# Performance work log

Hardware: AMD Instinct MI355X
Metric: run time of the kernel (lower is better)

## Reference

```python
import jax, jax.numpy as jnp
import numpy as np

B, CIN, COUT, G, HEADS = 4, 256, 256, 8, 4
K, S, P = 7, 1, 3
H = W = 32
IN_W = CIN // G
OUT_W = COUT // G


def setup_inputs() -> dict:
    key = jax.random.key(0)
    ks = jax.random.split(key, 9)
    def n(k, shape, scale=1.0):
        return jax.random.normal(k, shape, dtype=jnp.float32) * scale
    # kaiming fan_out init for the 1x1 convs (fan_out = out channels)
    return {
        "x": n(ks[0], (B, CIN, H, W)),
        "wq": n(ks[1], (G, OUT_W * HEADS, IN_W), (2.0 / (OUT_W * HEADS)) ** 0.5),
        "bq": n(ks[2], (G, OUT_W * HEADS), 0.01),
        "wk": n(ks[3], (G, OUT_W, IN_W), (2.0 / OUT_W) ** 0.5),
        "bk": n(ks[4], (G, OUT_W), 0.01),
        "wv": n(ks[5], (G, OUT_W, IN_W), (2.0 / OUT_W) ** 0.5),
        "bv": n(ks[6], (G, OUT_W), 0.01),
        "rel_h": n(ks[7], (OUT_W // 2, 1, 1, G, K, 1)),
        "rel_w": n(ks[8], (OUT_W // 2, 1, 1, G, 1, K)),
    }


def _sparse_conv(x, w, b):
    # grouped 1x1 conv, groups stacked on last axis (matches torch.stack(dim=-1))
    # x: [B, G*I, h, w]; w: [G, O, I]; b: [G, O] -> [B, O, h, w, G]
    Bn, C, hh, ww = x.shape
    xr = x.reshape(Bn, G, C // G, hh, ww)
    out = jnp.einsum('bgihw,goi->bohwg', xr, w)
    return out + b.T[None, :, None, None, :]


def _unfold(x5, k, s):
    # x5: [B, C, Hp, Wp, G] -> [B, C, Ho, Wo, G, k, k]  (torch unfold(2).unfold(3))
    Bn, C, Hp, Wp, Gn = x5.shape
    Ho = (Hp - k) // s + 1
    Wo = (Wp - k) // s + 1
    patches = jnp.stack(
        [x5[:, :, i:i + (Ho - 1) * s + 1:s, j:j + (Wo - 1) * s + 1:s, :]
         for i in range(k) for j in range(k)], axis=-1)
    return patches.reshape(Bn, C, Ho, Wo, Gn, k, k)


def reference(x, wq, bq, wk, bk, wv, bv, rel_h, rel_w):
    xp = jnp.pad(x, ((0, 0), (0, 0), (P, P), (P, P)))
    q = _sparse_conv(x, wq, bq)    # [B, OUT_W*HEADS, H, W, G]
    k = _sparse_conv(xp, wk, bk)   # [B, OUT_W, Hp, Wp, G] (bias at padded locations, as in torch)
    v = _sparse_conv(xp, wv, bv)
    k = _unfold(k, K, S)           # [B, OUT_W, H, W, G, K, K]
    v = _unfold(v, K, S)
    kh, kw = jnp.split(k, 2, axis=1)
    k = jnp.concatenate([kh + rel_h, kw + rel_w], axis=1)
    kf = k.reshape(B, OUT_W, H, W, G * K * K)
    vf = v.reshape(B, OUT_W, H, W, G * K * K)
    q = q.reshape(B, HEADS, OUT_W, H, W, G)
    # scores: sum over channel c; softmax over flattened (group, kh, kw) window
    scores = jnp.einsum('bhcxyg,bcxym->bhxygm', q, kf)
    attn = jax.nn.softmax(scores, axis=-1)
    # weighted sum over window m and heads h (matches sum(dim=1) then sum(dim=-1))
    out = jnp.einsum('bhxygm,bcxym->bcxyg', attn, vf)   # [B, OUT_W, H, W, G]
    out = jnp.transpose(out, (0, 4, 2, 3, 1)).reshape(B, -1, H, W)  # transpose(1,-1)+reshape
    return out
```

## Files before the change

### kernel.cpp

```cpp
#include <hip/hip_runtime.h>
#include <math.h>

typedef _Float16 f16;
typedef _Float16 f16x4 __attribute__((ext_vector_type(4)));
typedef _Float16 f16x8 __attribute__((ext_vector_type(8)));
typedef __bf16 bf16x4 __attribute__((ext_vector_type(4)));
typedef short s16x4 __attribute__((ext_vector_type(4)));
typedef float f32x4 __attribute__((ext_vector_type(4)));
typedef unsigned int u32;

#define MFMA_F16(a, b, c)  __builtin_amdgcn_mfma_f32_16x16x32_f16(a, b, c, 0, 0, 0)
#define MFMA_BF16_K16(a, b, c) __builtin_amdgcn_mfma_f32_16x16x16bf16_1k(a, b, c, 0, 0, 0)

static __device__ inline f16x8 cvt8(const float* p) {
    const float4* p4 = (const float4*)p;
    float4 u0 = p4[0], u1 = p4[1];
    f16x8 r;
    r[0] = (f16)u0.x; r[1] = (f16)u0.y; r[2] = (f16)u0.z; r[3] = (f16)u0.w;
    r[4] = (f16)u1.x; r[5] = (f16)u1.y; r[6] = (f16)u1.z; r[7] = (f16)u1.w;
    return r;
}

static __device__ inline u32 alignsel(u32 hi, u32 lo, u32 sh) {
    return sh ? (u32)(((((unsigned long long)hi) << 32) | lo) >> sh) : lo;
}

__global__ __launch_bounds__(512, 1) void fused_kernel(
    const float* __restrict__ x,
    const float* __restrict__ wq, const float* __restrict__ bq,
    const float* __restrict__ wk, const float* __restrict__ bk,
    const float* __restrict__ wv, const float* __restrict__ bv,
    const float* __restrict__ rel_h, const float* __restrict__ rel_w,
    float* __restrict__ out) {
    __shared__ __align__(16) f16 Klds[33600];
    __shared__ __align__(16) __bf16 Vlds[35840];
    __shared__ __align__(16) f16 Qlds[8192];
    __shared__ __align__(16) f16 TrwL[2048];

    int bid = blockIdx.x;
    int t = threadIdx.x;
    int G = (bid & 7) * 64 + (bid >> 3);
    int yq = G & 3, xx = (G >> 2) & 31, b = G >> 7;
    int y0 = yq * 8;
    int b8 = b * 8;

    int wvi = t >> 6;
    int lane = t & 63;
    int l15 = lane & 15, quad = lane >> 4, kwl = lane & 7, p8 = (lane >> 3) & 1;
    bool oddq = (quad & 1);

    {
        int g = wvi;

        const float* xb = x + ((size_t)(b * 256 + g * 32 + quad * 8) * 32) * 32;
        int cX = y0 - 3 + l15;
        bool cok = ((unsigned)cX < 32u);
        f16x8 xf[7];
#pragma unroll
        for (int rr = 0; rr < 7; ++rr) {
            int rX = xx - 3 + rr;
            bool ok = cok && ((unsigned)rX < 32u);
            int off = rX * 32 + cX;
#pragma unroll
            for (int j = 0; j < 8; ++j) {
                float v = ok ? xb[off + j * 1024] : 0.f;
                xf[rr][j] = (f16)v;
            }
        }

        for (int i = t; i < 2048; i += 512) {
            int c = i & 31, gw = i >> 5;
            int g2 = gw >> 3, kw = gw & 7;
            TrwL[i] = (f16)((c >= 16 && kw < 7) ? rel_w[(c - 16) * 56 + g2 * 7 + kw] : 0.f);
        }

        f16x8 wkf[2], wvf[2];
        float4 bk4[2], bv4[2];
#pragma unroll
        for (int ct = 0; ct < 2; ++ct) {
            wkf[ct] = cvt8(wk + ((size_t)g * 32 + ct * 16 + l15) * 32 + quad * 8);
            wvf[ct] = cvt8(wv + ((size_t)g * 32 + ct * 16 + l15) * 32 + quad * 8);
            bk4[ct] = *(const float4*)(bk + g * 32 + ct * 16 + quad * 4);
            bv4[ct] = *(const float4*)(bv + g * 32 + ct * 16 + quad * 4);
        }

#pragma unroll
        for (int rr = 0; rr < 7; ++rr) {
            float rh0 = rel_h[(quad * 4 + 0) * 56 + g * 7 + rr];
            float rh1 = rel_h[(quad * 4 + 1) * 56 + g * 7 + rr];
            float rh2 = rel_h[(quad * 4 + 2) * 56 + g * 7 + rr];
            float rh3 = rel_h[(quad * 4 + 3) * 56 + g * 7 + rr];
#pragma unroll
            for (int ct = 0; ct < 2; ++ct) {
                f32x4 z = {0.f, 0.f, 0.f, 0.f};
                f32x4 dK = MFMA_F16(wkf[ct], xf[rr], z);
                f32x4 dV = MFMA_F16(wvf[ct], xf[rr], z);
                f16x4 k4;
                k4[0] = (f16)(dK[0] + bk4[ct].x + (ct ? 0.f : rh0));
                k4[1] = (f16)(dK[1] + bk4[ct].y + (ct ? 0.f : rh1));
                k4[2] = (f16)(dK[2] + bk4[ct].z + (ct ? 0.f : rh2));
                k4[3] = (f16)(dK[3] + bk4[ct].w + (ct ? 0.f : rh3));
                if (l15 < 15)
                    *(f16x4*)(Klds + ((g * 7 + rr) * 15 + l15) * 40 + ct * 16 + quad * 4) = k4;
                int vrow = (g * 7 + rr) * 32 + ct * 16 + quad * 4;
                Vlds[(vrow + 0) * 20 + l15] = (__bf16)(dV[0] + bv4[ct].x);
                Vlds[(vrow + 1) * 20 + l15] = (__bf16)(dV[1] + bv4[ct].y);
                Vlds[(vrow + 2) * 20 + l15] = (__bf16)(dV[2] + bv4[ct].z);
                Vlds[(vrow + 3) * 20 + l15] = (__bf16)(dV[3] + bv4[ct].w);
            }
        }

#pragma unroll
        for (int mq = 0; mq < 8; ++mq) {
            f16x8 wqf = cvt8(wq + ((size_t)g * 128 + mq * 16 + l15) * 32 + quad * 8);
            float4 bq4 = *(const float4*)(bq + g * 128 + mq * 16 + quad * 4);
            f32x4 z = {0.f, 0.f, 0.f, 0.f};
            f32x4 d = MFMA_F16(wqf, xf[3], z);
            if (l15 >= 3 && l15 <= 10) {
                f16x4 q4;
                q4[0] = (f16)(d[0] + bq4.x); q4[1] = (f16)(d[1] + bq4.y);
                q4[2] = (f16)(d[2] + bq4.z); q4[3] = (f16)(d[3] + bq4.w);
                *(f16x4*)(Qlds + (l15 - 3) * 1024 + g * 128 + mq * 16 + quad * 4) = q4;
            }
        }
    }
    __syncthreads();

    int y = y0 + wvi;

    f16x8 qf[2];
    qf[0] = *(const f16x8*)(Qlds + wvi * 1024 + l15 * 32 + quad * 8);
    qf[1] = *(const f16x8*)(Qlds + wvi * 1024 + 512 + l15 * 32 + quad * 8);

    float fsumT[2] = {0.f, 0.f};
    f32x4 acc[2][2];
#pragma unroll
    for (int ct = 0; ct < 2; ++ct)
#pragma unroll
        for (int m = 0; m < 2; ++m) acc[ct][m] = (f32x4){0.f, 0.f, 0.f, 0.f};

    int wplk = wvi + kwl;
    u32 shsel = (wvi & 1) ? 16u : 0u;
    bool hi4 = (wvi & 2) != 0;
    int eA = ((quad & 1) + (wvi >> 2)) * 4;

#pragma unroll
    for (int chunk = 0; chunk < 4; ++chunk) {
        int gpr = chunk * 2 + p8;
        int gpv = chunk * 2 + (quad >> 1);
        f16x8 rp = *(const f16x8*)(TrwL + (gpr * 8 + kwl) * 32 + quad * 8);
        const f16* kp = Klds + (gpr * 105 + wplk) * 40 + quad * 8;
        const __bf16* vb0 = Vlds + (size_t)gpv * 4480 + l15 * 20 + eA;
        const __bf16* vb1 = vb0 + 320;
#pragma unroll
        for (int kh = 0; kh < 7; ++kh) {
            f16x8 kb = *(const f16x8*)kp;  kp += 600;
            kb += rp;
            uint2 A0 = *(const uint2*)vb0;
            uint2 B0 = *(const uint2*)(vb0 + 4);
            uint2 A1 = *(const uint2*)vb1;
            uint2 B1 = *(const uint2*)(vb1 + 4);
            vb0 += 640; vb1 += 640;
            u32 a0 = hi4 ? A0.y : A0.x, a1 = hi4 ? B0.x : A0.y, a2 = hi4 ? B0.y : B0.x;
            s16x4 vf0 = __builtin_bit_cast(s16x4,
                make_uint2(alignsel(a1, a0, shsel), alignsel(a2, a1, shsel)));
            u32 c0 = hi4 ? A1.y : A1.x, c1 = hi4 ? B1.x : A1.y, c2 = hi4 ? B1.y : B1.x;
            s16x4 vf1 = __builtin_bit_cast(s16x4,
                make_uint2(alignsel(c1, c0, shsel), alignsel(c2, c1, shsel)));
#pragma unroll
            for (int Mt = 0; Mt < 2; ++Mt) {
                f32x4 d = {0.f, 0.f, 0.f, 0.f};
                d = MFMA_F16(kb, qf[Mt], d);
                float e0 = __expf(d[0]);
                float e1 = __expf(d[1]);
                float e2 = __expf(d[2]);
                float e3 = oddq ? 0.f : __expf(d[3]);
                fsumT[Mt] += (e0 + e1) + (e2 + e3);
                bf16x4 pb;
                pb[0] = (__bf16)e0; pb[1] = (__bf16)e1;
                pb[2] = (__bf16)e2; pb[3] = (__bf16)e3;
                s16x4 pbi = __builtin_bit_cast(s16x4, pb);
                acc[0][Mt] = MFMA_BF16_K16(vf0, pbi, acc[0][Mt]);
                acc[1][Mt] = MFMA_BF16_K16(vf1, pbi, acc[1][Mt]);
            }
        }
    }

#pragma unroll
    for (int m = 0; m < 2; ++m) {
        fsumT[m] += __shfl_xor(fsumT[m], 16);
        fsumT[m] += __shfl_xor(fsumT[m], 32);
    }
    float inv[2] = {1.0f / fsumT[0], 1.0f / fsumT[1]};

#pragma unroll
    for (int Mt = 0; Mt < 2; ++Mt)
#pragma unroll
        for (int ct = 0; ct < 2; ++ct) {
            float v[4];
#pragma unroll
            for (int r = 0; r < 4; ++r) {
                v[r] = acc[ct][Mt][r] * inv[Mt];
                v[r] += __shfl_xor(v[r], 1);
                v[r] += __shfl_xor(v[r], 2);
            }
            if ((l15 & 3) == 0) {
                int g = Mt * 4 + (l15 >> 2);
                float4 o4 = {v[0], v[1], v[2], v[3]};
                *(float4*)(out + ((((size_t)(b8 + g) * 32 + xx) * 32 + y) << 5) +
                           ct * 16 + quad * 4) = o4;
            }
        }
}

extern "C" void kernel_launch(void* const* d_in, const int* in_sizes, int n_in,
                              void* d_out, int out_size, void* d_ws, size_t ws_size,
                              hipStream_t stream) {
    const float* x     = (const float*)d_in[0];
    const float* wq    = (const float*)d_in[1];
    const float* bq    = (const float*)d_in[2];
    const float* wk    = (const float*)d_in[3];
    const float* bk    = (const float*)d_in[4];
    const float* wv    = (const float*)d_in[5];
    const float* bv    = (const float*)d_in[6];
    const float* rel_h = (const float*)d_in[7];
    const float* rel_w = (const float*)d_in[8];
    float* out = (float*)d_out;
    (void)d_ws; (void)ws_size;

    hipLaunchKernelGGL(fused_kernel, dim3(512), dim3(512), 0, stream,
                       x, wq, bq, wk, bk, wv, bv, rel_h, rel_w, out);
}
```

Measured before the change: 131.1 us.

## Stream K/V window rows through smaller LDS buffers to raise occupancy

Instead of projecting all seven kernel rows of K and V into LDS before attention, the kernel now produces them in three phases (2, 3 and 2 rows) and runs the attention loop over each phase, reusing a much smaller LDS buffer. This cuts LDS use and register pressure (x rows are no longer all held in registers), and the launch bounds now ask for 4 blocks per CU so more blocks can be resident. In exchange it adds extra __syncthreads barriers between phases and serializes projection and attention within a block. The online softmax needs no rescaling because scores are exponentiated directly and normalized at the end.

New measurement: 147.5 us. 12.5% more time.

```diff
diff --git a/kernel.cpp b/kernel.cpp
--- a/kernel.cpp
+++ b/kernel.cpp
@@ -25,15 +25,15 @@
     return sh ? (u32)(((((unsigned long long)hi) << 32) | lo) >> sh) : lo;
 }
 
-__global__ __launch_bounds__(512, 1) void fused_kernel(
+__global__ __launch_bounds__(512, 4) void fused_kernel(
     const float* __restrict__ x,
     const float* __restrict__ wq, const float* __restrict__ bq,
     const float* __restrict__ wk, const float* __restrict__ bk,
     const float* __restrict__ wv, const float* __restrict__ bv,
     const float* __restrict__ rel_h, const float* __restrict__ rel_w,
     float* __restrict__ out) {
-    __shared__ __align__(16) f16 Klds[33600];
-    __shared__ __align__(16) __bf16 Vlds[35840];
+    __shared__ __align__(16) f16 Klds[14400];
+    __shared__ __align__(16) __bf16 Vlds[15360];
     __shared__ __align__(16) f16 Qlds[8192];
     __shared__ __align__(16) f16 TrwL[2048];
 
@@ -48,74 +48,142 @@
     int lane = t & 63;
     int l15 = lane & 15, quad = lane >> 4, kwl = lane & 7, p8 = (lane >> 3) & 1;
     bool oddq = (quad & 1);
-
+    int g = wvi;
+
+    f16x8 wkf0 = cvt8(wk + ((size_t)g * 32 + l15) * 32 + quad * 8);
+    f16x8 wkf1 = cvt8(wk + ((size_t)g * 32 + 16 + l15) * 32 + quad * 8);
+    f16x8 wvf0 = cvt8(wv + ((size_t)g * 32 + l15) * 32 + quad * 8);
+    f16x8 wvf1 = cvt8(wv + ((size_t)g * 32 + 16 + l15) * 32 + quad * 8);
+    float4 bk40 = *(const float4*)(bk + g * 32 + quad * 4);
+    float4 bk41 = *(const float4*)(bk + g * 32 + 16 + quad * 4);
+    float4 bv40 = *(const float4*)(bv + g * 32 + quad * 4);
+    float4 bv41 = *(const float4*)(bv + g * 32 + 16 + quad * 4);
+
+    const float* xb = x + ((size_t)(b * 256 + g * 32 + quad * 8) * 32) * 32;
+    int cX = y0 - 3 + l15;
+    bool cok = ((unsigned)cX < 32u);
+
+    auto prodRow = [&](int khs, int jrow, int rr) {
+        int rX = xx - 3 + rr;
+        bool ok = cok && ((unsigned)rX < 32u);
+        int off = rX * 32 + cX;
+        f16x8 xfr;
+#pragma unroll
+        for (int jj = 0; jj < 8; ++jj) {
+            float v = ok ? xb[off + jj * 1024] : 0.f;
+            xfr[jj] = (f16)v;
+        }
+        float rh0 = rel_h[(quad * 4 + 0) * 56 + g * 7 + rr];
+        float rh1 = rel_h[(quad * 4 + 1) * 56 + g * 7 + rr];
+        float rh2 = rel_h[(quad * 4 + 2) * 56 + g * 7 + rr];
+        float rh3 = rel_h[(quad * 4 + 3) * 56 + g * 7 + rr];
+        f32x4 z = {0.f, 0.f, 0.f, 0.f};
+        {
+            f32x4 dK = MFMA_F16(wkf0, xfr, z);
+            f32x4 dV = MFMA_F16(wvf0, xfr, z);
+            f16x4 k4;
+            k4[0] = (f16)(dK[0] + bk40.x + rh0);
+            k4[1] = (f16)(dK[1] + bk40.y + rh1);
+            k4[2] = (f16)(dK[2] + bk40.z + rh2);
+            k4[3] = (f16)(dK[3] + bk40.w + rh3);
+            if (l15 < 15)
+                *(f16x4*)(Klds + ((g * khs + jrow) * 15 + l15) * 40 + quad * 4) = k4;
+            int vrow = (g * khs + jrow) * 32 + quad * 4;
+            Vlds[(vrow + 0) * 20 + l15] = (__bf16)(dV[0] + bv40.x);
+            Vlds[(vrow + 1) * 20 + l15] = (__bf16)(dV[1] + bv40.y);
+            Vlds[(vrow + 2) * 20 + l15] = (__bf16)(dV[2] + bv40.z);
+            Vlds[(vrow + 3) * 20 + l15] = (__bf16)(dV[3] + bv40.w);
+        }
+        {
+            f32x4 dK = MFMA_F16(wkf1, xfr, z);
+            f32x4 dV = MFMA_F16(wvf1, xfr, z);
+            f16x4 k4;
+            k4[0] = (f16)(dK[0] + bk41.x);
+            k4[1] = (f16)(dK[1] + bk41.y);
+            k4[2] = (f16)(dK[2] + bk41.z);
+            k4[3] = (f16)(dK[3] + bk41.w);
+            if (l15 < 15)
+                *(f16x4*)(Klds + ((g * khs + jrow) * 15 + l15) * 40 + 16 + quad * 4) = k4;
+            int vrow = (g * khs + jrow) * 32 + 16 + quad * 4;
+            Vlds[(vrow + 0) * 20 + l15] = (__bf16)(dV[0] + bv41.x);
+            Vlds[(vrow + 1) * 20 + l15] = (__bf16)(dV[1] + bv41.y);
+            Vlds[(vrow + 2) * 20 + l15] = (__bf16)(dV[2] + bv41.z);
+            Vlds[(vrow + 3) * 20 + l15] = (__bf16)(dV[3] + bv41.w);
+        }
+    };
+
+    f16x8 qf[2];
+    float fsumT[2] = {0.f, 0.f};
+    f32x4 acc[2][2];
+#pragma unroll
+    for (int ct = 0; ct < 2; ++ct)
+#pragma unroll
+        for (int m = 0; m < 2; ++m) acc[ct][m] = (f32x4){0.f, 0.f, 0.f, 0.f};
+
+    int wplk = wvi + kwl;
+    u32 shsel = (wvi & 1) ? 16u : 0u;
+    bool hi4 = (wvi & 2) != 0;
+    int eA = ((quad & 1) + (wvi >> 2)) * 4;
+
+    auto attend = [&](int khs) {
+#pragma unroll
+        for (int chunk = 0; chunk < 4; ++chunk) {
+            int gpr = chunk * 2 + p8;
+            int gpv = chunk * 2 + (quad >> 1);
+            f16x8 rp = *(const f16x8*)(TrwL + (gpr * 8 + kwl) * 32 + quad * 8);
+            const f16* kp = Klds + ((gpr * khs) * 15 + wplk) * 40 + quad * 8;
+            const __bf16* vb0 = Vlds + ((gpv * khs) * 32 + l15) * 20 + eA;
+            const __bf16* vb1 = vb0 + 320;
+            for (int j = 0; j < khs; ++j) {
+                f16x8 kb = *(const f16x8*)kp;  kp += 600;
+                kb += rp;
+                uint2 A0 = *(const uint2*)vb0;
+                uint2 B0 = *(const uint2*)(vb0 + 4);
+                uint2 A1 = *(const uint2*)vb1;
+                uint2 B1 = *(const uint2*)(vb1 + 4);
+                vb0 += 640; vb1 += 640;
+                u32 a0 = hi4 ? A0.y : A0.x, a1 = hi4 ? B0.x : A0.y, a2 = hi4 ? B0.y : B0.x;
+                s16x4 vf0 = __builtin_bit_cast(s16x4,
+                    make_uint2(alignsel(a1, a0, shsel), alignsel(a2, a1, shsel)));
+                u32 c0 = hi4 ? A1.y : A1.x, c1 = hi4 ? B1.x : A1.y, c2 = hi4 ? B1.y : B1.x;
+                s16x4 vf1 = __builtin_bit_cast(s16x4,
+                    make_uint2(alignsel(c1, c0, shsel), alignsel(c2, c1, shsel)));
+#pragma unroll
+                for (int Mt = 0; Mt < 2; ++Mt) {
+                    f32x4 d = {0.f, 0.f, 0.f, 0.f};
+                    d = MFMA_F16(kb, qf[Mt], d);
+                    float e0 = __expf(d[0]);
+                    float e1 = __expf(d[1]);
+                    float e2 = __expf(d[2]);
+                    float e3 = oddq ? 0.f : __expf(d[3]);
+                    fsumT[Mt] += (e0 + e1) + (e2 + e3);
+                    bf16x4 pb;
+                    pb[0] = (__bf16)e0; pb[1] = (__bf16)e1;
+                    pb[2] = (__bf16)e2; pb[3] = (__bf16)e3;
+                    s16x4 pbi = __builtin_bit_cast(s16x4, pb);
+                    acc[0][Mt] = MFMA_BF16_K16(vf0, pbi, acc[0][Mt]);
+                    acc[1][Mt] = MFMA_BF16_K16(vf1, pbi, acc[1][Mt]);
+                }
+            }
+        }
+    };
+
+    prodRow(2, 0, 3);
+    prodRow(2, 1, 4);
     {
-        int g = wvi;
-
-        const float* xb = x + ((size_t)(b * 256 + g * 32 + quad * 8) * 32) * 32;
-        int cX = y0 - 3 + l15;
-        bool cok = ((unsigned)cX < 32u);
-        f16x8 xf[7];
-#pragma unroll
-        for (int rr = 0; rr < 7; ++rr) {
-            int rX = xx - 3 + rr;
-            bool ok = cok && ((unsigned)rX < 32u);
-            int off = rX * 32 + cX;
-#pragma unroll
-            for (int j = 0; j < 8; ++j) {
-                float v = ok ? xb[off + j * 1024] : 0.f;
-                xf[rr][j] = (f16)v;
-            }
-        }
-
-        for (int i = t; i < 2048; i += 512) {
-            int c = i & 31, gw = i >> 5;
-            int g2 = gw >> 3, kw = gw & 7;
-            TrwL[i] = (f16)((c >= 16 && kw < 7) ? rel_w[(c - 16) * 56 + g2 * 7 + kw] : 0.f);
-        }
-
-        f16x8 wkf[2], wvf[2];
-        float4 bk4[2], bv4[2];
-#pragma unroll
-        for (int ct = 0; ct < 2; ++ct) {
-            wkf[ct] = cvt8(wk + ((size_t)g * 32 + ct * 16 + l15) * 32 + quad * 8);
-            wvf[ct] = cvt8(wv + ((size_t)g * 32 + ct * 16 + l15) * 32 + quad * 8);
-            bk4[ct] = *(const float4*)(bk + g * 32 + ct * 16 + quad * 4);
-            bv4[ct] = *(const float4*)(bv + g * 32 + ct * 16 + quad * 4);
-        }
-
-#pragma unroll
-        for (int rr = 0; rr < 7; ++rr) {
-            float rh0 = rel_h[(quad * 4 + 0) * 56 + g * 7 + rr];
-            float rh1 = rel_h[(quad * 4 + 1) * 56 + g * 7 + rr];
-            float rh2 = rel_h[(quad * 4 + 2) * 56 + g * 7 + rr];
-            float rh3 = rel_h[(quad * 4 + 3) * 56 + g * 7 + rr];
-#pragma unroll
-            for (int ct = 0; ct < 2; ++ct) {
-                f32x4 z = {0.f, 0.f, 0.f, 0.f};
-                f32x4 dK = MFMA_F16(wkf[ct], xf[rr], z);
-                f32x4 dV = MFMA_F16(wvf[ct], xf[rr], z);
-                f16x4 k4;
-                k4[0] = (f16)(dK[0] + bk4[ct].x + (ct ? 0.f : rh0));
-                k4[1] = (f16)(dK[1] + bk4[ct].y + (ct ? 0.f : rh1));
-                k4[2] = (f16)(dK[2] + bk4[ct].z + (ct ? 0.f : rh2));
-                k4[3] = (f16)(dK[3] + bk4[ct].w + (ct ? 0.f : rh3));
-                if (l15 < 15)
-                    *(f16x4*)(Klds + ((g * 7 + rr) * 15 + l15) * 40 + ct * 16 + quad * 4) = k4;
-                int vrow = (g * 7 + rr) * 32 + ct * 16 + quad * 4;
-                Vlds[(vrow + 0) * 20 + l15] = (__bf16)(dV[0] + bv4[ct].x);
-                Vlds[(vrow + 1) * 20 + l15] = (__bf16)(dV[1] + bv4[ct].y);
-                Vlds[(vrow + 2) * 20 + l15] = (__bf16)(dV[2] + bv4[ct].z);
-                Vlds[(vrow + 3) * 20 + l15] = (__bf16)(dV[3] + bv4[ct].w);
-            }
-        }
-
+        int off = xx * 32 + cX;
+        f16x8 xq;
+#pragma unroll
+        for (int jj = 0; jj < 8; ++jj) {
+            float v = cok ? xb[off + jj * 1024] : 0.f;
+            xq[jj] = (f16)v;
+        }
 #pragma unroll
         for (int mq = 0; mq < 8; ++mq) {
             f16x8 wqf = cvt8(wq + ((size_t)g * 128 + mq * 16 + l15) * 32 + quad * 8);
             float4 bq4 = *(const float4*)(bq + g * 128 + mq * 16 + quad * 4);
             f32x4 z = {0.f, 0.f, 0.f, 0.f};
-            f32x4 d = MFMA_F16(wqf, xf[3], z);
+            f32x4 d = MFMA_F16(wqf, xq, z);
             if (l15 >= 3 && l15 <= 10) {
                 f16x4 q4;
                 q4[0] = (f16)(d[0] + bq4.x); q4[1] = (f16)(d[1] + bq4.y);
@@ -124,67 +192,28 @@
             }
         }
     }
-    __syncthreads();
-
-    int y = y0 + wvi;
-
-    f16x8 qf[2];
+    for (int i = t; i < 2048; i += 512) {
+        int c = i & 31, gw = i >> 5;
+        int g2 = gw >> 3, kw = gw & 7;
+        TrwL[i] = (f16)((c >= 16 && kw < 7) ? rel_w[(c - 16) * 56 + g2 * 7 + kw] : 0.f);
+    }
+    __syncthreads();
     qf[0] = *(const f16x8*)(Qlds + wvi * 1024 + l15 * 32 + quad * 8);
     qf[1] = *(const f16x8*)(Qlds + wvi * 1024 + 512 + l15 * 32 + quad * 8);
-
-    float fsumT[2] = {0.f, 0.f};
-    f32x4 acc[2][2];
-#pragma unroll
-    for (int ct = 0; ct < 2; ++ct)
-#pragma unroll
-        for (int m = 0; m < 2; ++m) acc[ct][m] = (f32x4){0.f, 0.f, 0.f, 0.f};
-
-    int wplk = wvi + kwl;
-    u32 shsel = (wvi & 1) ? 16u : 0u;
-    bool hi4 = (wvi & 2) != 0;
-    int eA = ((quad & 1) + (wvi >> 2)) * 4;
-
-#pragma unroll
-    for (int chunk = 0; chunk < 4; ++chunk) {
-        int gpr = chunk * 2 + p8;
-        int gpv = chunk * 2 + (quad >> 1);
-        f16x8 rp = *(const f16x8*)(TrwL + (gpr * 8 + kwl) * 32 + quad * 8);
-        const f16* kp = Klds + (gpr * 105 + wplk) * 40 + quad * 8;
-        const __bf16* vb0 = Vlds + (size_t)gpv * 4480 + l15 * 20 + eA;
-        const __bf16* vb1 = vb0 + 320;
-#pragma unroll
-        for (int kh = 0; kh < 7; ++kh) {
-            f16x8 kb = *(const f16x8*)kp;  kp += 600;
-            kb += rp;
-            uint2 A0 = *(const uint2*)vb0;
-            uint2 B0 = *(const uint2*)(vb0 + 4);
-            uint2 A1 = *(const uint2*)vb1;
-            uint2 B1 = *(const uint2*)(vb1 + 4);
-            vb0 += 640; vb1 += 640;
-            u32 a0 = hi4 ? A0.y : A0.x, a1 = hi4 ? B0.x : A0.y, a2 = hi4 ? B0.y : B0.x;
-            s16x4 vf0 = __builtin_bit_cast(s16x4,
-                make_uint2(alignsel(a1, a0, shsel), alignsel(a2, a1, shsel)));
-            u32 c0 = hi4 ? A1.y : A1.x, c1 = hi4 ? B1.x : A1.y, c2 = hi4 ? B1.y : B1.x;
-            s16x4 vf1 = __builtin_bit_cast(s16x4,
-                make_uint2(alignsel(c1, c0, shsel), alignsel(c2, c1, shsel)));
-#pragma unroll
-            for (int Mt = 0; Mt < 2; ++Mt) {
-                f32x4 d = {0.f, 0.f, 0.f, 0.f};
-                d = MFMA_F16(kb, qf[Mt], d);
-                float e0 = __expf(d[0]);
-                float e1 = __expf(d[1]);
-                float e2 = __expf(d[2]);
-                float e3 = oddq ? 0.f : __expf(d[3]);
-                fsumT[Mt] += (e0 + e1) + (e2 + e3);
-                bf16x4 pb;
-                pb[0] = (__bf16)e0; pb[1] = (__bf16)e1;
-                pb[2] = (__bf16)e2; pb[3] = (__bf16)e3;
-                s16x4 pbi = __builtin_bit_cast(s16x4, pb);
-                acc[0][Mt] = MFMA_BF16_K16(vf0, pbi, acc[0][Mt]);
-                acc[1][Mt] = MFMA_BF16_K16(vf1, pbi, acc[1][Mt]);
-            }
-        }
-    }
+    attend(2);
+    __syncthreads();
+
+    prodRow(3, 0, 0);
+    prodRow(3, 1, 1);
+    prodRow(3, 2, 2);
+    __syncthreads();
+    attend(3);
+    __syncthreads();
+
+    prodRow(2, 0, 5);
+    prodRow(2, 1, 6);
+    __syncthreads();
+    attend(2);
 
 #pragma unroll
     for (int m = 0; m < 2; ++m) {
@@ -193,6 +222,7 @@
     }
     float inv[2] = {1.0f / fsumT[0], 1.0f / fsumT[1]};
 
+    int y = y0 + wvi;
 #pragma unroll
     for (int Mt = 0; Mt < 2; ++Mt)
 #pragma unroll
@@ -205,9 +235,9 @@
                 v[r] += __shfl_xor(v[r], 2);
             }
             if ((l15 & 3) == 0) {
-                int g = Mt * 4 + (l15 >> 2);
+                int go = Mt * 4 + (l15 >> 2);
                 float4 o4 = {v[0], v[1], v[2], v[3]};
-                *(float4*)(out + ((((size_t)(b8 + g) * 32 + xx) * 32 + y) << 5) +
+                *(float4*)(out + ((((size_t)(b8 + go) * 32 + xx) * 32 + y) << 5) +
                            ct * 16 + quad * 4) = o4;
             }
         }
```
